# Performance work log

Hardware: AMD Instinct MI355X
Metric: run time of the kernel (lower is better)

The kernel has to match this reference:

```python
import jax, jax.numpy as jnp
import numpy as np

B, S, D, H = 2, 2048, 1024, 16
HD = D // H  # head_dim = 64
LN_EPS = 1e-5


def setup_inputs() -> dict:
    key = jax.random.key(0)
    ks = jax.random.split(key, 14)
    w = 0.02  # weight init scale
    return {
        "q": jax.random.normal(ks[0], (B, S, D), jnp.float32),
        "k": jax.random.normal(ks[1], (B, S, D), jnp.float32),
        "v": jax.random.normal(ks[2], (B, S, D), jnp.float32),
        "mask": jnp.zeros((B, 1, S, S), dtype=bool),
        "training": 0,
        "wq_w": jax.random.normal(ks[3], (D, D), jnp.float32) * w,
        "wq_b": jnp.zeros((D,), jnp.float32),
        "wk_w": jax.random.normal(ks[4], (D, D), jnp.float32) * w,
        "wk_b": jnp.zeros((D,), jnp.float32),
        "wv_w": jax.random.normal(ks[5], (D, D), jnp.float32) * w,
        "wv_b": jnp.zeros((D,), jnp.float32),
        "wo_w": jax.random.normal(ks[6], (D, D), jnp.float32) * w,
        "wo_b": jnp.zeros((D,), jnp.float32),
        "ln_g": jnp.ones((D,), jnp.float32),
        "ln_b": jnp.zeros((D,), jnp.float32),
    }


def _linear(x, w, b):
    # torch nn.Linear: x @ W.T + b, W is [out, in]
    return jnp.einsum('bsd,od->bso', x, w) + b


def _split_heads(x):
    b, s, _ = x.shape
    return x.reshape(b, s, H, HD).transpose(0, 2, 1, 3)  # [B,H,S,HD]


def reference(q, k, v, mask, training, wq_w, wq_b, wk_w, wk_b, wv_w, wv_b,
              wo_w, wo_b, ln_g, ln_b):
    residual = q
    Q = _split_heads(_linear(q, wq_w, wq_b))
    K = _split_heads(_linear(k, wk_w, wk_b))
    V = _split_heads(_linear(v, wv_w, wv_b))
    # source computes sqrt(dk) in float16, then adds 1e-8
    dk = jnp.sqrt(jnp.asarray(HD, jnp.float16)).astype(jnp.float32) + 1e-8
    score = jnp.einsum('bhqd,bhkd->bhqk', Q, K) / dk  # [B,H,S,S]
    # NOTE: source applies NO softmax; masked score is used directly.
    attn = jnp.where(mask, -jnp.inf, score)
    ctx = jnp.einsum('bhqk,bhkd->bhqd', attn, V)  # [B,H,S,HD]
    b, _, s, _ = ctx.shape
    ctx = ctx.transpose(0, 2, 1, 3).reshape(b, s, D)  # [B,S,D]
    o = _linear(ctx, wo_w, wo_b)
    # dropout is identity in eval mode
    x = residual + o
    mu = jnp.mean(x, axis=-1, keepdims=True)
    var = jnp.mean(jnp.square(x - mu), axis=-1, keepdims=True)
    return ln_g * (x - mu) * jax.lax.rsqrt(var + LN_EPS) + ln_b
```

## Files before the change

kernel.cpp:

```cpp
#include <hip/hip_runtime.h>


typedef __bf16 bf16;
typedef __bf16 bf16x4 __attribute__((ext_vector_type(4)));
typedef __bf16 bf16x8 __attribute__((ext_vector_type(8)));
typedef float f32x4 __attribute__((ext_vector_type(4)));

#define MFMA16(a, b, c) __builtin_amdgcn_mfma_f32_16x16x32_bf16(a, b, c, 0, 0, 0)
#define BARRIER() asm volatile("s_barrier" ::: "memory")
#define VMCNT4() asm volatile("s_waitcnt vmcnt(4)" ::: "memory")
#define VMCNT0() asm volatile("s_waitcnt vmcnt(0)" ::: "memory")
#define LGKM0()                                        \
  do {                                                 \
    asm volatile("s_waitcnt lgkmcnt(0)" ::: "memory"); \
    __builtin_amdgcn_sched_barrier(0);                 \
  } while (0)

__device__ __forceinline__ bf16x8 ld8(const bf16* p) { return *(const bf16x8*)p; }

__device__ __forceinline__ void gload16(const void* g, void* l) {
  __builtin_amdgcn_global_load_lds((__attribute__((address_space(1))) void*)(g),
                                   (__attribute__((address_space(3))) void*)(l), 16, 0, 0);
}

__device__ __forceinline__ int swz4(int row) { return (row ^ (row >> 2)) & 3; }

__device__ __forceinline__ bf16x8 cvt8(f32x4 lo, f32x4 hi) {
  bf16x8 o;
  o[0] = (bf16)lo[0]; o[1] = (bf16)lo[1]; o[2] = (bf16)lo[2]; o[3] = (bf16)lo[3];
  o[4] = (bf16)hi[0]; o[5] = (bf16)hi[1]; o[6] = (bf16)hi[2]; o[7] = (bf16)hi[3];
  return o;
}

__device__ __forceinline__ void compute16(const char* buf, const int aoff[4], const int boff[4],
                                          f32x4 (&acc)[4][4]) {
  bf16x8 av[4], bv[4];
#pragma unroll
  for (int i = 0; i < 4; i++) av[i] = *(const bf16x8*)(buf + aoff[i]);
#pragma unroll
  for (int j = 0; j < 4; j++) bv[j] = *(const bf16x8*)(buf + boff[j]);
  __builtin_amdgcn_s_setprio(1);
#pragma unroll
  for (int i = 0; i < 4; i++)
#pragma unroll
    for (int j = 0; j < 4; j++) acc[i][j] = MFMA16(av[i], bv[j], acc[i][j]);
  __builtin_amdgcn_s_setprio(0);
}

__device__ __forceinline__ void ring128(const bf16* __restrict__ A, const bf16* __restrict__ B,
                                        char* lds, f32x4 (&acc)[4][4]) {
  const int t = threadIdx.x;
  const int lane = t & 63, wid = t >> 6;
  const int wr = wid >> 1, wc = wid & 1;
  const int r16 = lane & 15, kg = lane >> 4;

  int aoff[4], boff[4];
#pragma unroll
  for (int i = 0; i < 4; i++) {
    int row = wr * 64 + i * 16 + r16;
    aoff[i] = row * 64 + ((kg ^ swz4(row)) << 4);
    row = wc * 64 + i * 16 + r16;
    boff[i] = 8192 + row * 64 + ((kg ^ swz4(row)) << 4);
  }

  const int r1 = t >> 2, c = t & 3, r2 = r1 + 64;
  const bf16* pa1 = A + (size_t)r1 * 1024 + (c ^ swz4(r1)) * 8;
  const bf16* pa2 = A + (size_t)r2 * 1024 + (c ^ swz4(r2)) * 8;
  const bf16* pb1 = B + (size_t)r1 * 1024 + (c ^ swz4(r1)) * 8;
  const bf16* pb2 = B + (size_t)r2 * 1024 + (c ^ swz4(r2)) * 8;
  const int d1 = wid << 10, d2 = 4096 + (wid << 10);

#pragma unroll
  for (int p = 0; p < 2; p++) {
    char* d = lds + p * 16384;
    gload16(pa1 + p * 32, d + d1);
    gload16(pa2 + p * 32, d + d2);
    gload16(pb1 + p * 32, d + 8192 + d1);
    gload16(pb2 + p * 32, d + 8192 + d2);
  }
  pa1 += 64; pa2 += 64; pb1 += 64; pb2 += 64;

  int cb = 0, rb = 2;
  for (int kt = 0; kt < 30; kt++) {
    VMCNT4();
    BARRIER();
    {
      char* d = lds + rb * 16384;
      gload16(pa1, d + d1);
      gload16(pa2, d + d2);
      gload16(pb1, d + 8192 + d1);
      gload16(pb2, d + 8192 + d2);
      pa1 += 32; pa2 += 32; pb1 += 32; pb2 += 32;
    }
    compute16(lds + cb * 16384, aoff, boff, acc);
    LGKM0();
    cb = (cb == 2) ? 0 : cb + 1;
    rb = (rb == 2) ? 0 : rb + 1;
  }
  VMCNT4(); BARRIER();
  compute16(lds + cb * 16384, aoff, boff, acc);
  LGKM0();
  cb = (cb == 2) ? 0 : cb + 1;
  VMCNT0(); BARRIER();
  compute16(lds + cb * 16384, aoff, boff, acc);
}

__device__ __forceinline__ void proj_epi(f32x4 (&acc)[4][4], const float* bias,
                                         bf16* __restrict__ C, int m0, int n0) {
  const int lane = threadIdx.x & 63, wid = threadIdx.x >> 6;
  const int wr = wid >> 1, wc = wid & 1, r16 = lane & 15, kg = lane >> 4;
#pragma unroll
  for (int j = 0; j < 4; j++) {
    const int col = n0 + wc * 64 + j * 16 + r16;
    const float bj = bias[col];
#pragma unroll
    for (int i = 0; i < 4; i++) {
      const int row = m0 + wr * 64 + i * 16 + kg * 4;
#pragma unroll
      for (int r = 0; r < 4; r++)
        C[(size_t)(row + r) * 1024 + col] = (bf16)(acc[i][j][r] + bj);
    }
  }
}

__global__ __launch_bounds__(256) void cvt_kvw_kernel(
    const float* __restrict__ k, const float* __restrict__ v,
    const float* __restrict__ wk, const float* __restrict__ wv,
    bf16* __restrict__ kv_bf, bf16* __restrict__ wkv_bf, float* __restrict__ Mz) {
  const int bid = blockIdx.x;
  if (bid >= 5120) {
    float* p = Mz + (size_t)(bid - 5120) * 2048 + threadIdx.x * 8;
    *(f32x4*)p = f32x4{0.f, 0.f, 0.f, 0.f};
    *(f32x4*)(p + 4) = f32x4{0.f, 0.f, 0.f, 0.f};
    return;
  }
  const float* s; bf16* d; size_t dof; int x;
  if (bid < 4096) {
    const int y = bid >> 11; x = bid & 2047;
    s = (y == 0) ? k : v;
    d = kv_bf; dof = (size_t)y * 4194304u;
  } else {
    const int idx = bid - 4096; const int y = idx >> 9; x = idx & 511;
    s = (y == 0) ? wk : wv;
    d = wkv_bf; dof = (size_t)y * 1048576u;
  }
  const size_t i = ((size_t)x * 256 + threadIdx.x) * 8;
  *(bf16x8*)(d + dof + i) = cvt8(*(const f32x4*)(s + i), *(const f32x4*)(s + i + 4));
}

__global__ __launch_bounds__(256, 2) void fat_a_kernel(
    const bf16* __restrict__ kv_bf, const bf16* __restrict__ wkv,
    const float* __restrict__ bk, const float* __restrict__ bv_, float* __restrict__ Mout,
    const float* __restrict__ q, const float* __restrict__ wq,
    bf16* __restrict__ q_bf, bf16* __restrict__ wq_bf) {
  __shared__ __align__(1024) char lds[49152];
  const int wg = blockIdx.x;
  if (wg < 256) {
    const int swz = (wg & 7) * 32 + (wg >> 3);
    const int mt = swz >> 3, nt = swz & 7;
    const int m0 = mt * 128, n0 = nt * 128;
    const int b = mt >> 4;

    f32x4 accK[4][4] = {}, accV[4][4] = {};
    ring128(kv_bf + (size_t)m0 * 1024, wkv + (size_t)n0 * 1024, lds, accK);
    __syncthreads();
    ring128(kv_bf + 4194304u + (size_t)m0 * 1024, wkv + 1048576u + (size_t)n0 * 1024,
            lds, accV);
    __syncthreads();

    bf16 (*Kl)[136] = (bf16(*)[136])lds;
    bf16 (*Vl)[136] = (bf16(*)[136])(lds + 17408);
    const int lane = threadIdx.x & 63, wid = threadIdx.x >> 6;
    const int wr = wid >> 1, wc = wid & 1, r16 = lane & 15, kg = lane >> 4;
#pragma unroll
    for (int g = 0; g < 2; ++g) {
      if (g) __syncthreads();
      if (wc == g) {
#pragma unroll
        for (int j = 0; j < 4; j++) {
          const int col = n0 + g * 64 + j * 16 + r16;
          const float bkj = bk[col], bvj = bv_[col];
#pragma unroll
          for (int i = 0; i < 4; i++) {
            const int sb = wr * 64 + i * 16 + kg * 4;
            bf16x4 pk, pv;
#pragma unroll
            for (int r = 0; r < 4; r++) {
              pk[r] = (bf16)(accK[i][j][r] + bkj);
              pv[r] = (bf16)(accV[i][j][r] + bvj);
            }
            *(bf16x4*)&Kl[j * 16 + r16][sb] = pk;
            *(bf16x4*)&Vl[j * 16 + r16][sb] = pv;
          }
        }
      }
      __syncthreads();
      f32x4 accm[4] = {};
#pragma unroll
      for (int ks = 0; ks < 4; ks++) {
        bf16x8 a = ld8(&Kl[wid * 16 + r16][ks * 32 + kg * 8]);
#pragma unroll
        for (int j = 0; j < 4; j++) {
          bf16x8 bb = ld8(&Vl[j * 16 + r16][ks * 32 + kg * 8]);
          accm[j] = MFMA16(a, bb, accm[j]);
        }
      }
      float* Mh = Mout + (size_t)(b * 16 + nt * 2 + g) * 4096;
#pragma unroll
      for (int j = 0; j < 4; j++)
#pragma unroll
        for (int r = 0; r < 4; r++)
          atomicAdd(&Mh[(wid * 16 + kg * 4 + r) * 64 + j * 16 + r16], accm[j][r]);
    }
    return;
  }
  const int idx = wg - 256;
  const float* s; bf16* d; int x;
  if (idx < 2048) { s = q; d = q_bf; x = idx; }
  else            { s = wq; d = wq_bf; x = idx - 2048; }
  const size_t i = ((size_t)x * 256 + threadIdx.x) * 8;
  *(bf16x8*)(d + i) = cvt8(*(const f32x4*)(s + i), *(const f32x4*)(s + i + 4));
}

__global__ __launch_bounds__(256, 3) void fat_b_kernel(
    const bf16* __restrict__ q_bf, const bf16* __restrict__ wq_bf,
    const float* __restrict__ bq, bf16* __restrict__ Q_bf,
    const float* __restrict__ Wo, const float* __restrict__ M, bf16* __restrict__ Gt) {
  __shared__ __align__(1024) char lds[49152];
  const int wg = blockIdx.x;
  if (wg < 256) {
    const int swz = (wg & 7) * 32 + (wg >> 3);
    const int mt = swz >> 3, nt = swz & 7;
    const int m0 = mt * 128, n0 = nt * 128;
    f32x4 acc[4][4] = {};
    ring128(q_bf + (size_t)m0 * 1024, wq_bf + (size_t)n0 * 1024, lds, acc);
    proj_epi(acc, bq, Q_bf, m0, n0);
    return;
  }
  const int bid = wg - 256;
  const int b = bid >> 7, h = (bid >> 3) & 15, nt = bid & 7;
  const int n0 = nt * 128;
  const float* Mh = M + (size_t)((b << 4) + h) * 4096;
  const int l = threadIdx.x & 63, w = threadIdx.x >> 6;
  const int r16 = l & 15, kg = l >> 4;
  f32x4 acc[2][4] = {};
#pragma unroll
  for (int kk = 0; kk < 2; kk++) {
    bf16x8 a[2];
#pragma unroll
    for (int i = 0; i < 2; i++) {
      const float* wp = Wo + (size_t)(n0 + w * 32 + i * 16 + r16) * 1024 + h * 64 + kk * 32 + kg * 8;
      a[i] = cvt8(*(const f32x4*)wp, *(const f32x4*)(wp + 4));
    }
#pragma unroll
    for (int j = 0; j < 4; j++) {
      const float* mp = Mh + (j * 16 + r16) * 64 + kk * 32 + kg * 8;
      f32x4 m0v = *(const f32x4*)mp;
      f32x4 m1v = *(const f32x4*)(mp + 4);
      f32x4 sl = {m0v[0] * 0.125f, m0v[1] * 0.125f, m0v[2] * 0.125f, m0v[3] * 0.125f};
      f32x4 sh = {m1v[0] * 0.125f, m1v[1] * 0.125f, m1v[2] * 0.125f, m1v[3] * 0.125f};
      bf16x8 bv = cvt8(sl, sh);
#pragma unroll
      for (int i = 0; i < 2; i++) acc[i][j] = MFMA16(a[i], bv, acc[i][j]);
    }
  }
  bf16* G = Gt + (size_t)b * 1048576u;
#pragma unroll
  for (int i = 0; i < 2; i++)
#pragma unroll
    for (int j = 0; j < 4; j++)
#pragma unroll
      for (int r = 0; r < 4; r++)
        G[(size_t)(n0 + w * 32 + i * 16 + kg * 4 + r) * 1024 + h * 64 + j * 16 + r16] =
            (bf16)acc[i][j][r];
}

__global__ __launch_bounds__(256, 3) void gemm_out_r(
    const bf16* __restrict__ Q, const bf16* __restrict__ Gt,
    const float* __restrict__ bo, const float* __restrict__ resid, bf16* __restrict__ xb) {
  __shared__ __align__(1024) char lds[49152];
  const int wg = blockIdx.x;
  const int swz = (wg & 7) * 32 + (wg >> 3);
  const int mt = swz >> 3, nt = swz & 7;
  const int m0 = mt * 128, n0 = nt * 128;

  f32x4 acc[4][4] = {};
  ring128(Q + (size_t)m0 * 1024, Gt + (size_t)(m0 >> 11) * 1048576u + (size_t)n0 * 1024, lds, acc);

  const int lane = threadIdx.x & 63, wid = threadIdx.x >> 6;
  const int wr = wid >> 1, wc = wid & 1, r16 = lane & 15, kg = lane >> 4;
#pragma unroll
  for (int j = 0; j < 4; j++) {
    const int col = n0 + wc * 64 + j * 16 + r16;
    const float bj = bo[col];
#pragma unroll
    for (int i = 0; i < 4; i++) {
      const int row = m0 + wr * 64 + i * 16 + kg * 4;
#pragma unroll
      for (int r = 0; r < 4; r++) {
        const size_t off = (size_t)(row + r) * 1024 + col;
        xb[off] = (bf16)(acc[i][j][r] + bj + resid[off]);
      }
    }
  }
}

__global__ __launch_bounds__(256) void ln_kernel(
    const bf16* __restrict__ xb, const float* __restrict__ g, const float* __restrict__ bb,
    float* __restrict__ out) {
  const int lane = threadIdx.x & 63, wid = threadIdx.x >> 6;
  const int row = (blockIdx.x << 2) + wid;
  const bf16* xr = xb + (size_t)row * 1024;
  bf16x8 h0 = ld8(xr + lane * 16);
  bf16x8 h1 = ld8(xr + lane * 16 + 8);
  float v[16];
#pragma unroll
  for (int e = 0; e < 8; e++) { v[e] = (float)h0[e]; v[8 + e] = (float)h1[e]; }
  float s = 0.f, s2 = 0.f;
#pragma unroll
  for (int e = 0; e < 16; e++) { s += v[e]; s2 += v[e] * v[e]; }
#pragma unroll
  for (int m = 32; m; m >>= 1) { s += __shfl_xor(s, m); s2 += __shfl_xor(s2, m); }
  const float mu = s * (1.0f / 1024.0f);
  const float rstd = rsqrtf(s2 * (1.0f / 1024.0f) - mu * mu + 1e-5f);
  float* orow = out + (size_t)row * 1024 + lane * 16;
#pragma unroll
  for (int e = 0; e < 4; e++) {
    f32x4 gg = *(const f32x4*)(g + lane * 16 + e * 4);
    f32x4 bv = *(const f32x4*)(bb + lane * 16 + e * 4);
    f32x4 o;
#pragma unroll
    for (int u = 0; u < 4; u++) o[u] = gg[u] * ((v[e * 4 + u] - mu) * rstd) + bv[u];
    *(f32x4*)(orow + e * 4) = o;
  }
}

extern "C" void kernel_launch(void* const* d_in, const int* in_sizes, int n_in,
                              void* d_out, int out_size, void* d_ws, size_t ws_size,
                              hipStream_t stream) {
  (void)in_sizes; (void)n_in; (void)out_size; (void)ws_size;
  const float* q    = (const float*)d_in[0];
  const float* k    = (const float*)d_in[1];
  const float* v    = (const float*)d_in[2];
  const float* wq_w = (const float*)d_in[5];
  const float* wq_b = (const float*)d_in[6];
  const float* wk_w = (const float*)d_in[7];
  const float* wk_b = (const float*)d_in[8];
  const float* wv_w = (const float*)d_in[9];
  const float* wv_b = (const float*)d_in[10];
  const float* wo_w = (const float*)d_in[11];
  const float* wo_b = (const float*)d_in[12];
  const float* ln_g = (const float*)d_in[13];
  const float* ln_b = (const float*)d_in[14];
  float* out = (float*)d_out;

  bf16* wsb    = (bf16*)d_ws;
  bf16* q_bf   = wsb;
  bf16* kv_bf  = wsb + 4194304u;
  bf16* w_bf   = wsb + 12582912u;
  bf16* Q_bf   = wsb + 15728640u;
  bf16* Gt     = wsb + 19922944u;
  bf16* xb     = wsb + 22020096u;
  float* M     = (float*)(wsb + 28311552u);

  cvt_kvw_kernel<<<5184, 256, 0, stream>>>(k, v, wk_w, wv_w, kv_bf, w_bf + 1048576u, M);
  fat_a_kernel<<<2816, 256, 0, stream>>>(kv_bf, w_bf + 1048576u, wk_b, wv_b, M,
                                         q, wq_w, q_bf, w_bf);
  fat_b_kernel<<<512, 256, 0, stream>>>(q_bf, w_bf, wq_b, Q_bf, wo_w, M, Gt);
  gemm_out_r<<<256, 256, 0, stream>>>(Q_bf, Gt, wo_b, q, xb);
  ln_kernel<<<1024, 256, 0, stream>>>(xb, ln_g, ln_b, out);
}
```

Before: 91.97 us.

## Split K/V projection tiles to 128x64 with triple-buffered ring to double workgroups

The fused K/V projection plus per-head K^T V reduction now uses 128x64 output tiles, one per head, instead of 128x128 tiles covering two heads. A new ring64 loader triple-buffers 64-wide K slices in 72KB of LDS. This doubles the number of GEMM workgroups from 256 to 512, which should fill the CUs better, and removes the serialized two-head epilogue loop. In exchange, each A tile is reloaded twice as often, and the larger LDS footprint may lower occupancy below the declared two blocks per CU.

```diff
diff --git a/kernel.cpp b/kernel.cpp
--- a/kernel.cpp
+++ b/kernel.cpp
@@ -8,6 +8,7 @@
 
 #define MFMA16(a, b, c) __builtin_amdgcn_mfma_f32_16x16x32_bf16(a, b, c, 0, 0, 0)
 #define BARRIER() asm volatile("s_barrier" ::: "memory")
+#define VMCNT6() asm volatile("s_waitcnt vmcnt(6)" ::: "memory")
 #define VMCNT4() asm volatile("s_waitcnt vmcnt(4)" ::: "memory")
 #define VMCNT0() asm volatile("s_waitcnt vmcnt(0)" ::: "memory")
 #define LGKM0()                                        \
@@ -123,6 +124,86 @@
   }
 }
 
+__device__ __forceinline__ void ring64(const bf16* __restrict__ A, const bf16* __restrict__ B,
+                                       char* lds, f32x4 (&acc)[4][2]) {
+  const int t = threadIdx.x;
+  const int lane = t & 63, wid = t >> 6;
+  const int wr = wid >> 1, wc = wid & 1;
+  const int r16 = lane & 15, kg = lane >> 4;
+
+  int aoff[4][2], boff[2][2];
+#pragma unroll
+  for (int i = 0; i < 4; i++) {
+    const int row = wr * 64 + i * 16 + r16;
+#pragma unroll
+    for (int kk = 0; kk < 2; kk++)
+      aoff[i][kk] = row * 128 + (((kk * 4 + kg) ^ (row & 7)) << 4);
+  }
+#pragma unroll
+  for (int j = 0; j < 2; j++) {
+    const int row = wc * 32 + j * 16 + r16;
+#pragma unroll
+    for (int kk = 0; kk < 2; kk++)
+      boff[j][kk] = 16384 + row * 128 + (((kk * 4 + kg) ^ (row & 7)) << 4);
+  }
+
+  const bf16* pa[4]; const bf16* pb[2];
+  int adst[4], bdst[2];
+#pragma unroll
+  for (int p = 0; p < 4; p++) {
+    const int slot = p * 256 + t;
+    const int row = slot >> 3, c = slot & 7;
+    pa[p] = A + (size_t)row * 1024 + (c ^ (row & 7)) * 8;
+    adst[p] = p * 4096 + (wid << 10);
+  }
+#pragma unroll
+  for (int p = 0; p < 2; p++) {
+    const int slot = p * 256 + t;
+    const int row = slot >> 3, c = slot & 7;
+    pb[p] = B + (size_t)row * 1024 + (c ^ (row & 7)) * 8;
+    bdst[p] = 16384 + p * 4096 + (wid << 10);
+  }
+
+#pragma unroll
+  for (int kt0 = 0; kt0 < 2; kt0++) {
+    char* d = lds + kt0 * 24576;
+#pragma unroll
+    for (int p = 0; p < 4; p++) gload16(pa[p] + kt0 * 64, d + adst[p]);
+#pragma unroll
+    for (int p = 0; p < 2; p++) gload16(pb[p] + kt0 * 64, d + bdst[p]);
+  }
+
+  int cb = 0;
+  for (int kt = 0; kt < 16; ++kt) {
+    if (kt < 14) VMCNT6(); else if (kt == 14) VMCNT6(); else VMCNT0();
+    BARRIER();
+    if (kt < 14) {
+      char* d = lds + ((kt + 2) % 3) * 24576;
+#pragma unroll
+      for (int p = 0; p < 4; p++) gload16(pa[p] + (kt + 2) * 64, d + adst[p]);
+#pragma unroll
+      for (int p = 0; p < 2; p++) gload16(pb[p] + (kt + 2) * 64, d + bdst[p]);
+    }
+    const char* buf = lds + cb * 24576;
+#pragma unroll
+    for (int kk = 0; kk < 2; kk++) {
+      bf16x8 av[4], bv[2];
+#pragma unroll
+      for (int i = 0; i < 4; i++) av[i] = *(const bf16x8*)(buf + aoff[i][kk]);
+#pragma unroll
+      for (int j = 0; j < 2; j++) bv[j] = *(const bf16x8*)(buf + boff[j][kk]);
+      __builtin_amdgcn_s_setprio(1);
+#pragma unroll
+      for (int i = 0; i < 4; i++)
+#pragma unroll
+        for (int j = 0; j < 2; j++) acc[i][j] = MFMA16(av[i], bv[j], acc[i][j]);
+      __builtin_amdgcn_s_setprio(0);
+    }
+    LGKM0();
+    cb = (cb == 2) ? 0 : cb + 1;
+  }
+}
+
 __global__ __launch_bounds__(256) void cvt_kvw_kernel(
     const float* __restrict__ k, const float* __restrict__ v,
     const float* __restrict__ wk, const float* __restrict__ wv,
@@ -148,24 +229,24 @@
   *(bf16x8*)(d + dof + i) = cvt8(*(const f32x4*)(s + i), *(const f32x4*)(s + i + 4));
 }
 
-__global__ __launch_bounds__(256, 2) void fat_a_kernel(
+__global__ __launch_bounds__(256, 2) void fat_a2_kernel(
     const bf16* __restrict__ kv_bf, const bf16* __restrict__ wkv,
     const float* __restrict__ bk, const float* __restrict__ bv_, float* __restrict__ Mout,
     const float* __restrict__ q, const float* __restrict__ wq,
     bf16* __restrict__ q_bf, bf16* __restrict__ wq_bf) {
-  __shared__ __align__(1024) char lds[49152];
+  __shared__ __align__(1024) char lds[73728];
   const int wg = blockIdx.x;
-  if (wg < 256) {
-    const int swz = (wg & 7) * 32 + (wg >> 3);
-    const int mt = swz >> 3, nt = swz & 7;
-    const int m0 = mt * 128, n0 = nt * 128;
+  if (wg < 512) {
+    const int swz = (wg & 7) * 64 + (wg >> 3);
+    const int mt = swz >> 4, nt = swz & 15;
+    const int m0 = mt * 128;
     const int b = mt >> 4;
 
-    f32x4 accK[4][4] = {}, accV[4][4] = {};
-    ring128(kv_bf + (size_t)m0 * 1024, wkv + (size_t)n0 * 1024, lds, accK);
+    f32x4 accK[4][2] = {}, accV[4][2] = {};
+    ring64(kv_bf + (size_t)m0 * 1024, wkv + (size_t)nt * 64 * 1024, lds, accK);
     __syncthreads();
-    ring128(kv_bf + 4194304u + (size_t)m0 * 1024, wkv + 1048576u + (size_t)n0 * 1024,
-            lds, accV);
+    ring64(kv_bf + 4194304u + (size_t)m0 * 1024, wkv + 1048576u + (size_t)nt * 64 * 1024,
+           lds, accV);
     __syncthreads();
 
     bf16 (*Kl)[136] = (bf16(*)[136])lds;
@@ -173,48 +254,43 @@
     const int lane = threadIdx.x & 63, wid = threadIdx.x >> 6;
     const int wr = wid >> 1, wc = wid & 1, r16 = lane & 15, kg = lane >> 4;
 #pragma unroll
-    for (int g = 0; g < 2; ++g) {
-      if (g) __syncthreads();
-      if (wc == g) {
-#pragma unroll
-        for (int j = 0; j < 4; j++) {
-          const int col = n0 + g * 64 + j * 16 + r16;
-          const float bkj = bk[col], bvj = bv_[col];
-#pragma unroll
-          for (int i = 0; i < 4; i++) {
-            const int sb = wr * 64 + i * 16 + kg * 4;
-            bf16x4 pk, pv;
-#pragma unroll
-            for (int r = 0; r < 4; r++) {
-              pk[r] = (bf16)(accK[i][j][r] + bkj);
-              pv[r] = (bf16)(accV[i][j][r] + bvj);
-            }
-            *(bf16x4*)&Kl[j * 16 + r16][sb] = pk;
-            *(bf16x4*)&Vl[j * 16 + r16][sb] = pv;
-          }
+    for (int j = 0; j < 2; j++) {
+      const int d = wc * 32 + j * 16 + r16;
+      const int col = nt * 64 + d;
+      const float bkj = bk[col], bvj = bv_[col];
+#pragma unroll
+      for (int i = 0; i < 4; i++) {
+        const int sb = wr * 64 + i * 16 + kg * 4;
+        bf16x4 pk, pv;
+#pragma unroll
+        for (int r = 0; r < 4; r++) {
+          pk[r] = (bf16)(accK[i][j][r] + bkj);
+          pv[r] = (bf16)(accV[i][j][r] + bvj);
         }
+        *(bf16x4*)&Kl[d][sb] = pk;
+        *(bf16x4*)&Vl[d][sb] = pv;
       }
-      __syncthreads();
-      f32x4 accm[4] = {};
-#pragma unroll
-      for (int ks = 0; ks < 4; ks++) {
-        bf16x8 a = ld8(&Kl[wid * 16 + r16][ks * 32 + kg * 8]);
-#pragma unroll
-        for (int j = 0; j < 4; j++) {
-          bf16x8 bb = ld8(&Vl[j * 16 + r16][ks * 32 + kg * 8]);
-          accm[j] = MFMA16(a, bb, accm[j]);
-        }
+    }
+    __syncthreads();
+    f32x4 accm[4] = {};
+#pragma unroll
+    for (int ks = 0; ks < 4; ks++) {
+      bf16x8 a = ld8(&Kl[wid * 16 + r16][ks * 32 + kg * 8]);
+#pragma unroll
+      for (int j = 0; j < 4; j++) {
+        bf16x8 bb = ld8(&Vl[j * 16 + r16][ks * 32 + kg * 8]);
+        accm[j] = MFMA16(a, bb, accm[j]);
       }
-      float* Mh = Mout + (size_t)(b * 16 + nt * 2 + g) * 4096;
-#pragma unroll
-      for (int j = 0; j < 4; j++)
-#pragma unroll
-        for (int r = 0; r < 4; r++)
-          atomicAdd(&Mh[(wid * 16 + kg * 4 + r) * 64 + j * 16 + r16], accm[j][r]);
-    }
+    }
+    float* Mh = Mout + (size_t)(b * 16 + nt) * 4096;
+#pragma unroll
+    for (int j = 0; j < 4; j++)
+#pragma unroll
+      for (int r = 0; r < 4; r++)
+        atomicAdd(&Mh[(wid * 16 + kg * 4 + r) * 64 + j * 16 + r16], accm[j][r]);
     return;
   }
-  const int idx = wg - 256;
+  const int idx = wg - 512;
   const float* s; bf16* d; int x;
   if (idx < 2048) { s = q; d = q_bf; x = idx; }
   else            { s = wq; d = wq_bf; x = idx - 2048; }
@@ -222,7 +298,7 @@
   *(bf16x8*)(d + i) = cvt8(*(const f32x4*)(s + i), *(const f32x4*)(s + i + 4));
 }
 
-__global__ __launch_bounds__(256, 3) void fat_b_kernel(
+__global__ __launch_bounds__(256, 3) void fat_b2_kernel(
     const bf16* __restrict__ q_bf, const bf16* __restrict__ wq_bf,
     const float* __restrict__ bq, bf16* __restrict__ Q_bf,
     const float* __restrict__ Wo, const float* __restrict__ M, bf16* __restrict__ Gt) {
@@ -364,9 +440,9 @@
   float* M     = (float*)(wsb + 28311552u);
 
   cvt_kvw_kernel<<<5184, 256, 0, stream>>>(k, v, wk_w, wv_w, kv_bf, w_bf + 1048576u, M);
-  fat_a_kernel<<<2816, 256, 0, stream>>>(kv_bf, w_bf + 1048576u, wk_b, wv_b, M,
-                                         q, wq_w, q_bf, w_bf);
-  fat_b_kernel<<<512, 256, 0, stream>>>(q_bf, w_bf, wq_b, Q_bf, wo_w, M, Gt);
+  fat_a2_kernel<<<3072, 256, 0, stream>>>(kv_bf, w_bf + 1048576u, wk_b, wv_b, M,
+                                          q, wq_w, q_bf, w_bf);
+  fat_b2_kernel<<<512, 256, 0, stream>>>(q_bf, w_bf, wq_b, Q_bf, wo_w, M, Gt);
   gemm_out_r<<<256, 256, 0, stream>>>(Q_bf, Gt, wo_b, q, xb);
   ln_kernel<<<1024, 256, 0, stream>>>(xb, ln_g, ln_b, out);
 }
```

Result: faster. 85.98 us, median of 2 (-6.5%).

## Halve K/V projection tile rows to 64 with a triple-buffered ring and higher occupancy

Applied to the files above, without the earlier changes.

The K/V projection plus K^T·V fusion in the first fat kernel now uses 64x128 tiles instead of 128x128. A new triple-buffered 64-row GEMM ring feeds it, and LDS drops to 36 KB so the launch bound can rise to 4 blocks per CU. The grid doubles to 512 GEMM workgroups, which fills the CUs better and raises occupancy. The trade-off is twice as many atomicAdd reductions into M and more reloading of the weight tiles.

```diff
diff --git a/kernel.cpp b/kernel.cpp
--- a/kernel.cpp
+++ b/kernel.cpp
@@ -9,6 +9,7 @@
 #define MFMA16(a, b, c) __builtin_amdgcn_mfma_f32_16x16x32_bf16(a, b, c, 0, 0, 0)
 #define BARRIER() asm volatile("s_barrier" ::: "memory")
 #define VMCNT4() asm volatile("s_waitcnt vmcnt(4)" ::: "memory")
+#define VMCNT3() asm volatile("s_waitcnt vmcnt(3)" ::: "memory")
 #define VMCNT0() asm volatile("s_waitcnt vmcnt(0)" ::: "memory")
 #define LGKM0()                                        \
   do {                                                 \
@@ -123,6 +124,72 @@
   }
 }
 
+__device__ __forceinline__ void ring64b(const bf16* __restrict__ A, const bf16* __restrict__ B,
+                                        char* lds, f32x4 (&acc)[2][4]) {
+  const int t = threadIdx.x;
+  const int lane = t & 63, wid = t >> 6;
+  const int wr = wid >> 1, wc = wid & 1;
+  const int r16 = lane & 15, kg = lane >> 4;
+
+  int aoff[2], boff[4];
+#pragma unroll
+  for (int i = 0; i < 2; i++) {
+    const int row = wr * 32 + i * 16 + r16;
+    aoff[i] = row * 64 + ((kg ^ swz4(row)) << 4);
+  }
+#pragma unroll
+  for (int j = 0; j < 4; j++) {
+    const int row = wc * 64 + j * 16 + r16;
+    boff[j] = 4096 + row * 64 + ((kg ^ swz4(row)) << 4);
+  }
+
+  const int ar = t >> 2, ac = t & 3;
+  const bf16* pa = A + (size_t)ar * 1024 + (ac ^ swz4(ar)) * 8;
+  const int adst = wid << 10;
+  const bf16* pb[2]; int bdst[2];
+#pragma unroll
+  for (int p = 0; p < 2; p++) {
+    const int slot = p * 256 + t;
+    const int row = slot >> 2, c = slot & 3;
+    pb[p] = B + (size_t)row * 1024 + (c ^ swz4(row)) * 8;
+    bdst[p] = 4096 + p * 4096 + (wid << 10);
+  }
+
+#pragma unroll
+  for (int kt0 = 0; kt0 < 2; kt0++) {
+    char* d = lds + kt0 * 12288;
+    gload16(pa + kt0 * 32, d + adst);
+    gload16(pb[0] + kt0 * 32, d + bdst[0]);
+    gload16(pb[1] + kt0 * 32, d + bdst[1]);
+  }
+
+  int cb = 0;
+  for (int kt = 0; kt < 32; ++kt) {
+    if (kt < 31) VMCNT3(); else VMCNT0();
+    BARRIER();
+    if (kt < 30) {
+      char* d = lds + ((kt + 2) % 3) * 12288;
+      gload16(pa + (kt + 2) * 32, d + adst);
+      gload16(pb[0] + (kt + 2) * 32, d + bdst[0]);
+      gload16(pb[1] + (kt + 2) * 32, d + bdst[1]);
+    }
+    const char* buf = lds + cb * 12288;
+    bf16x8 av[2], bv[4];
+#pragma unroll
+    for (int i = 0; i < 2; i++) av[i] = *(const bf16x8*)(buf + aoff[i]);
+#pragma unroll
+    for (int j = 0; j < 4; j++) bv[j] = *(const bf16x8*)(buf + boff[j]);
+    __builtin_amdgcn_s_setprio(1);
+#pragma unroll
+    for (int i = 0; i < 2; i++)
+#pragma unroll
+      for (int j = 0; j < 4; j++) acc[i][j] = MFMA16(av[i], bv[j], acc[i][j]);
+    __builtin_amdgcn_s_setprio(0);
+    LGKM0();
+    cb = (cb == 2) ? 0 : cb + 1;
+  }
+}
+
 __global__ __launch_bounds__(256) void cvt_kvw_kernel(
     const float* __restrict__ k, const float* __restrict__ v,
     const float* __restrict__ wk, const float* __restrict__ wv,
@@ -148,28 +215,28 @@
   *(bf16x8*)(d + dof + i) = cvt8(*(const f32x4*)(s + i), *(const f32x4*)(s + i + 4));
 }
 
-__global__ __launch_bounds__(256, 2) void fat_a_kernel(
+__global__ __launch_bounds__(256, 4) void fat_a3_kernel(
     const bf16* __restrict__ kv_bf, const bf16* __restrict__ wkv,
     const float* __restrict__ bk, const float* __restrict__ bv_, float* __restrict__ Mout,
     const float* __restrict__ q, const float* __restrict__ wq,
     bf16* __restrict__ q_bf, bf16* __restrict__ wq_bf) {
-  __shared__ __align__(1024) char lds[49152];
+  __shared__ __align__(1024) char lds[36864];
   const int wg = blockIdx.x;
-  if (wg < 256) {
-    const int swz = (wg & 7) * 32 + (wg >> 3);
-    const int mt = swz >> 3, nt = swz & 7;
-    const int m0 = mt * 128, n0 = nt * 128;
-    const int b = mt >> 4;
-
-    f32x4 accK[4][4] = {}, accV[4][4] = {};
-    ring128(kv_bf + (size_t)m0 * 1024, wkv + (size_t)n0 * 1024, lds, accK);
+  if (wg < 512) {
+    const int swz = (wg & 7) * 64 + (wg >> 3);
+    const int mt = swz >> 3, ntp = swz & 7;
+    const int m0 = mt * 64;
+    const int b = mt >> 5;
+
+    f32x4 accK[2][4] = {}, accV[2][4] = {};
+    ring64b(kv_bf + (size_t)m0 * 1024, wkv + (size_t)ntp * 131072u, lds, accK);
     __syncthreads();
-    ring128(kv_bf + 4194304u + (size_t)m0 * 1024, wkv + 1048576u + (size_t)n0 * 1024,
+    ring64b(kv_bf + 4194304u + (size_t)m0 * 1024, wkv + 1048576u + (size_t)ntp * 131072u,
             lds, accV);
     __syncthreads();
 
-    bf16 (*Kl)[136] = (bf16(*)[136])lds;
-    bf16 (*Vl)[136] = (bf16(*)[136])(lds + 17408);
+    bf16 (*Kl)[72] = (bf16(*)[72])lds;
+    bf16 (*Vl)[72] = (bf16(*)[72])(lds + 9216);
     const int lane = threadIdx.x & 63, wid = threadIdx.x >> 6;
     const int wr = wid >> 1, wc = wid & 1, r16 = lane & 15, kg = lane >> 4;
 #pragma unroll
@@ -178,26 +245,27 @@
       if (wc == g) {
 #pragma unroll
         for (int j = 0; j < 4; j++) {
-          const int col = n0 + g * 64 + j * 16 + r16;
+          const int dcol = j * 16 + r16;
+          const int col = ntp * 128 + g * 64 + dcol;
           const float bkj = bk[col], bvj = bv_[col];
 #pragma unroll
-          for (int i = 0; i < 4; i++) {
-            const int sb = wr * 64 + i * 16 + kg * 4;
+          for (int i = 0; i < 2; i++) {
+            const int sb = wr * 32 + i * 16 + kg * 4;
             bf16x4 pk, pv;
 #pragma unroll
             for (int r = 0; r < 4; r++) {
               pk[r] = (bf16)(accK[i][j][r] + bkj);
               pv[r] = (bf16)(accV[i][j][r] + bvj);
             }
-            *(bf16x4*)&Kl[j * 16 + r16][sb] = pk;
-            *(bf16x4*)&Vl[j * 16 + r16][sb] = pv;
+            *(bf16x4*)&Kl[dcol][sb] = pk;
+            *(bf16x4*)&Vl[dcol][sb] = pv;
           }
         }
       }
       __syncthreads();
       f32x4 accm[4] = {};
 #pragma unroll
-      for (int ks = 0; ks < 4; ks++) {
+      for (int ks = 0; ks < 2; ks++) {
         bf16x8 a = ld8(&Kl[wid * 16 + r16][ks * 32 + kg * 8]);
 #pragma unroll
         for (int j = 0; j < 4; j++) {
@@ -205,7 +273,7 @@
           accm[j] = MFMA16(a, bb, accm[j]);
         }
       }
-      float* Mh = Mout + (size_t)(b * 16 + nt * 2 + g) * 4096;
+      float* Mh = Mout + (size_t)(b * 16 + ntp * 2 + g) * 4096;
 #pragma unroll
       for (int j = 0; j < 4; j++)
 #pragma unroll
@@ -214,7 +282,7 @@
     }
     return;
   }
-  const int idx = wg - 256;
+  const int idx = wg - 512;
   const float* s; bf16* d; int x;
   if (idx < 2048) { s = q; d = q_bf; x = idx; }
   else            { s = wq; d = wq_bf; x = idx - 2048; }
@@ -222,7 +290,7 @@
   *(bf16x8*)(d + i) = cvt8(*(const f32x4*)(s + i), *(const f32x4*)(s + i + 4));
 }
 
-__global__ __launch_bounds__(256, 3) void fat_b_kernel(
+__global__ __launch_bounds__(256, 3) void fat_b2_kernel(
     const bf16* __restrict__ q_bf, const bf16* __restrict__ wq_bf,
     const float* __restrict__ bq, bf16* __restrict__ Q_bf,
     const float* __restrict__ Wo, const float* __restrict__ M, bf16* __restrict__ Gt) {
@@ -364,9 +432,9 @@
   float* M     = (float*)(wsb + 28311552u);
 
   cvt_kvw_kernel<<<5184, 256, 0, stream>>>(k, v, wk_w, wv_w, kv_bf, w_bf + 1048576u, M);
-  fat_a_kernel<<<2816, 256, 0, stream>>>(kv_bf, w_bf + 1048576u, wk_b, wv_b, M,
-                                         q, wq_w, q_bf, w_bf);
-  fat_b_kernel<<<512, 256, 0, stream>>>(q_bf, w_bf, wq_b, Q_bf, wo_w, M, Gt);
+  fat_a3_kernel<<<3072, 256, 0, stream>>>(kv_bf, w_bf + 1048576u, wk_b, wv_b, M,
+                                          q, wq_w, q_bf, w_bf);
+  fat_b2_kernel<<<512, 256, 0, stream>>>(q_bf, w_bf, wq_b, Q_bf, wo_w, M, Gt);
   gemm_out_r<<<256, 256, 0, stream>>>(Q_bf, Gt, wo_b, q, xb);
   ln_kernel<<<1024, 256, 0, stream>>>(xb, ln_g, ln_b, out);
 }
```

Measured after the change: 99.50 us. 8.2% more time.
